# Performance work log

Hardware: AMD Instinct MI355X
Metric: run time of the kernel (lower is better)

## Reference

```python
import jax, jax.numpy as jnp
import numpy as np

B, E, NODE, M, N = 1024, 128, 128, 128, 512


def setup_inputs() -> dict:
    key = jax.random.key(0)
    k = jax.random.split(key, 7)
    s = 1.0 / np.sqrt(E)
    sn = 1.0 / np.sqrt(NODE)
    return {
        "h_v": jax.random.normal(k[0], (B, NODE, N), dtype=jnp.float32),
        "h_w": jax.random.normal(k[1], (B, NODE, N), dtype=jnp.float32),
        "e_vw": jax.random.normal(k[2], (B, E, N), dtype=jnp.float32),
        "W_e": jax.random.uniform(k[3], (M, E), jnp.float32, -s, s),
        "b_e": jax.random.uniform(k[4], (M,), jnp.float32, -s, s),
        "W_h": jax.random.uniform(k[5], (M, NODE), jnp.float32, -sn, sn),
        "b_h": jax.random.uniform(k[6], (M,), jnp.float32, -sn, sn),
    }


def reference(h_v, h_w, e_vw, W_e, b_e, W_h, b_h):
    # m_linear: message[:,:,n] = Linear_e(e_vw[:,:,n]) + Linear_h(h_w[:,:,n])
    # Vectorized over all nodes at once. Output: [B, M, N]
    msg = jnp.einsum('ben,me->bmn', e_vw, W_e) + jnp.einsum('bfn,mf->bmn', h_w, W_h)
    return msg + (b_e + b_h)[None, :, None]
```

## Files before the change

### kernel.cpp

```cpp
#include <hip/hip_runtime.h>


typedef __bf16 bf16x8 __attribute__((ext_vector_type(8)));
typedef float  f32x4  __attribute__((ext_vector_type(4)));

#define NDIM   512
#define MDIM   128
#define NCHUNK 64
#define KLD    264

__global__ __launch_bounds__(256) void msg_kernel(
    const float* __restrict__ h_w,
    const float* __restrict__ e_vw,
    const float* __restrict__ W_e,
    const float* __restrict__ b_e,
    const float* __restrict__ W_h,
    const float* __restrict__ b_h,
    float* __restrict__ out)
{
  __shared__ __align__(16) __bf16 Xs[NCHUNK][KLD];

  const int b    = blockIdx.x;
  const int tid  = threadIdx.x;
  const int lane = tid & 63;
  const int wave = tid >> 6;
  const int l15  = lane & 15;
  const int quad = lane >> 4;
  const int mbase = wave * 32;

  bf16x8 afrag[2][8];
#pragma unroll
  for (int mt = 0; mt < 2; ++mt) {
    const int m = mbase + mt * 16 + l15;
#pragma unroll
    for (int ks = 0; ks < 8; ++ks) {
      const int k0 = ks * 32 + quad * 8;
      const float* src = (k0 < 128) ? (W_e + m * 128 + k0)
                                    : (W_h + m * 128 + (k0 - 128));
      f32x4 lo = *(const f32x4*)(src);
      f32x4 hi = *(const f32x4*)(src + 4);
      bf16x8 f;
      f[0] = (__bf16)lo[0]; f[1] = (__bf16)lo[1];
      f[2] = (__bf16)lo[2]; f[3] = (__bf16)lo[3];
      f[4] = (__bf16)hi[0]; f[5] = (__bf16)hi[1];
      f[6] = (__bf16)hi[2]; f[7] = (__bf16)hi[3];
      afrag[mt][ks] = f;
    }
  }

  float bias[2][4];
#pragma unroll
  for (int mt = 0; mt < 2; ++mt)
#pragma unroll
    for (int r = 0; r < 4; ++r) {
      const int m = mbase + mt * 16 + quad * 4 + r;
      bias[mt][r] = b_e[m] + b_h[m];
    }

  const int krow0 = wave * 64;
  const float* src_base = (wave < 2)
      ? (e_vw + ((size_t)b * 128 + krow0) * NDIM)
      : (h_w  + ((size_t)b * 128 + (krow0 - 128)) * NDIM);

  float* outb = out + (size_t)b * MDIM * NDIM;
  const f32x4 fzero = {0.f, 0.f, 0.f, 0.f};

  for (int c = 0; c < 8; ++c) {
    const int n0 = c * NCHUNK;

#pragma unroll 2
    for (int g = 0; g < 8; ++g) {
      const float* p = src_base + (size_t)(g * 8) * NDIM + n0 + lane;
      float t[8];
#pragma unroll
      for (int j = 0; j < 8; ++j) t[j] = p[(size_t)j * NDIM];
      bf16x8 v;
#pragma unroll
      for (int j = 0; j < 8; ++j) v[j] = (__bf16)t[j];
      *(bf16x8*)&Xs[lane][krow0 + g * 8] = v;
    }
    __syncthreads();

    f32x4 acc[2][4];
#pragma unroll
    for (int mt = 0; mt < 2; ++mt)
#pragma unroll
      for (int nt = 0; nt < 4; ++nt)
        acc[mt][nt] = fzero;

#pragma unroll
    for (int ks = 0; ks < 8; ++ks) {
      bf16x8 bfrag[4];
#pragma unroll
      for (int nt = 0; nt < 4; ++nt)
        bfrag[nt] = *(const bf16x8*)&Xs[nt * 16 + l15][ks * 32 + quad * 8];
#pragma unroll
      for (int mt = 0; mt < 2; ++mt)
#pragma unroll
        for (int nt = 0; nt < 4; ++nt)
          acc[mt][nt] = __builtin_amdgcn_mfma_f32_16x16x32_bf16(
              afrag[mt][ks], bfrag[nt], acc[mt][nt], 0, 0, 0);
    }

#pragma unroll
    for (int mt = 0; mt < 2; ++mt)
#pragma unroll
      for (int nt = 0; nt < 4; ++nt)
#pragma unroll
        for (int r = 0; r < 4; ++r) {
          const int m = mbase + mt * 16 + quad * 4 + r;
          outb[(size_t)m * NDIM + n0 + nt * 16 + l15] = acc[mt][nt][r] + bias[mt][r];
        }
    __syncthreads();
  }
}

extern "C" void kernel_launch(void* const* d_in, const int* in_sizes, int n_in,
                              void* d_out, int out_size, void* d_ws, size_t ws_size,
                              hipStream_t stream) {
  const float* h_w  = (const float*)d_in[1];
  const float* e_vw = (const float*)d_in[2];
  const float* W_e  = (const float*)d_in[3];
  const float* b_e  = (const float*)d_in[4];
  const float* W_h  = (const float*)d_in[5];
  const float* b_h  = (const float*)d_in[6];
  float* out = (float*)d_out;

  msg_kernel<<<dim3(1024), dim3(256), 0, stream>>>(h_w, e_vw, W_e, b_e, W_h, b_h, out);
}
```

Before: 701.4 us.

## Swap MFMA operand roles: weights in swizzled LDS, activations loaded straight into registers

Restructures the kernel so that each 512-thread block handles a 128-column slice of one batch. Each lane loads its activation column directly from global memory into bf16 B fragments, with no LDS staging and no per-chunk barriers. The weight matrix is staged once per block into XOR-swizzled LDS to avoid bank conflicts, and output goes out through nontemporal stores. The grid grows to four times as many blocks for more parallelism. The trade-off is that every block now re-converts the full 64KB weight matrix, and each thread keeps 64 floats of activations live in registers.

```diff
diff --git a/kernel.cpp b/kernel.cpp
--- a/kernel.cpp
+++ b/kernel.cpp
@@ -4,12 +4,9 @@
 typedef __bf16 bf16x8 __attribute__((ext_vector_type(8)));
 typedef float  f32x4  __attribute__((ext_vector_type(4)));
 
-#define NDIM   512
-#define MDIM   128
-#define NCHUNK 64
-#define KLD    264
+#define NDIM 512
 
-__global__ __launch_bounds__(256) void msg_kernel(
+__global__ __launch_bounds__(512, 4) void msg_kernel(
     const float* __restrict__ h_w,
     const float* __restrict__ e_vw,
     const float* __restrict__ W_e,
@@ -18,100 +15,81 @@
     const float* __restrict__ b_h,
     float* __restrict__ out)
 {
-  __shared__ __align__(16) __bf16 Xs[NCHUNK][KLD];
+  __shared__ __align__(16) __bf16 Ws[128 * 256];
 
-  const int b    = blockIdx.x;
   const int tid  = threadIdx.x;
   const int lane = tid & 63;
   const int wave = tid >> 6;
   const int l15  = lane & 15;
   const int quad = lane >> 4;
-  const int mbase = wave * 32;
 
-  bf16x8 afrag[2][8];
+  const int b    = blockIdx.x >> 2;
+  const int nq   = blockIdx.x & 3;
+  const int ncol = nq * 128 + wave * 16 + l15;
+
+  const float* pe = e_vw + ((size_t)b * 128 + quad * 8) * NDIM + ncol;
+  const float* ph = h_w  + ((size_t)b * 128 + quad * 8) * NDIM + ncol;
+  float xs[8][8];
 #pragma unroll
-  for (int mt = 0; mt < 2; ++mt) {
-    const int m = mbase + mt * 16 + l15;
+  for (int s = 0; s < 4; ++s)
 #pragma unroll
-    for (int ks = 0; ks < 8; ++ks) {
-      const int k0 = ks * 32 + quad * 8;
-      const float* src = (k0 < 128) ? (W_e + m * 128 + k0)
-                                    : (W_h + m * 128 + (k0 - 128));
-      f32x4 lo = *(const f32x4*)(src);
-      f32x4 hi = *(const f32x4*)(src + 4);
-      bf16x8 f;
-      f[0] = (__bf16)lo[0]; f[1] = (__bf16)lo[1];
-      f[2] = (__bf16)lo[2]; f[3] = (__bf16)lo[3];
-      f[4] = (__bf16)hi[0]; f[5] = (__bf16)hi[1];
-      f[6] = (__bf16)hi[2]; f[7] = (__bf16)hi[3];
-      afrag[mt][ks] = f;
-    }
+    for (int j = 0; j < 8; ++j)
+      xs[s][j] = pe[(size_t)(s * 32 + j) * NDIM];
+#pragma unroll
+  for (int s = 0; s < 4; ++s)
+#pragma unroll
+    for (int j = 0; j < 8; ++j)
+      xs[4 + s][j] = ph[(size_t)(s * 32 + j) * NDIM];
+
+#pragma unroll
+  for (int i = 0; i < 4; ++i) {
+    const int A = i * 512 + tid;
+    const int m = A >> 4, a = A & 15;
+    f32x4 lo = *(const f32x4*)(W_e + A * 8);
+    f32x4 hi = *(const f32x4*)(W_e + A * 8 + 4);
+    bf16x8 v;
+    v[0]=(__bf16)lo[0]; v[1]=(__bf16)lo[1]; v[2]=(__bf16)lo[2]; v[3]=(__bf16)lo[3];
+    v[4]=(__bf16)hi[0]; v[5]=(__bf16)hi[1]; v[6]=(__bf16)hi[2]; v[7]=(__bf16)hi[3];
+    *(bf16x8*)&Ws[m * 256 + ((a ^ (m & 7)) * 8)] = v;
+  }
+#pragma unroll
+  for (int i = 0; i < 4; ++i) {
+    const int A = i * 512 + tid;
+    const int m = A >> 4, a = 16 + (A & 15);
+    f32x4 lo = *(const f32x4*)(W_h + A * 8);
+    f32x4 hi = *(const f32x4*)(W_h + A * 8 + 4);
+    bf16x8 v;
+    v[0]=(__bf16)lo[0]; v[1]=(__bf16)lo[1]; v[2]=(__bf16)lo[2]; v[3]=(__bf16)lo[3];
+    v[4]=(__bf16)hi[0]; v[5]=(__bf16)hi[1]; v[6]=(__bf16)hi[2]; v[7]=(__bf16)hi[3];
+    *(bf16x8*)&Ws[m * 256 + ((a ^ (m & 7)) * 8)] = v;
+  }
+  __syncthreads();
+
+  bf16x8 bfrag[8];
+#pragma unroll
+  for (int s = 0; s < 8; ++s) {
+#pragma unroll
+    for (int j = 0; j < 8; ++j) bfrag[s][j] = (__bf16)xs[s][j];
   }
 
-  float bias[2][4];
+  float* outp = out + (size_t)b * 128 * NDIM + ncol;
 #pragma unroll
-  for (int mt = 0; mt < 2; ++mt)
+  for (int mt = 0; mt < 8; ++mt) {
+    f32x4 acc = {0.f, 0.f, 0.f, 0.f};
+    const int m  = mt * 16 + l15;
+    const int sw = m & 7;
+#pragma unroll
+    for (int s = 0; s < 8; ++s) {
+      bf16x8 af = *(const bf16x8*)&Ws[m * 256 + (((s * 4 + quad) ^ sw) * 8)];
+      acc = __builtin_amdgcn_mfma_f32_16x16x32_bf16(af, bfrag[s], acc, 0, 0, 0);
+    }
+    f32x4 be = *(const f32x4*)(b_e + mt * 16 + quad * 4);
+    f32x4 bh = *(const f32x4*)(b_h + mt * 16 + quad * 4);
 #pragma unroll
     for (int r = 0; r < 4; ++r) {
-      const int m = mbase + mt * 16 + quad * 4 + r;
-      bias[mt][r] = b_e[m] + b_h[m];
+      __builtin_nontemporal_store(acc[r] + be[r] + bh[r],
+          outp + (size_t)(mt * 16 + quad * 4 + r) * NDIM);
     }
-
-  const int krow0 = wave * 64;
-  const float* src_base = (wave < 2)
-      ? (e_vw + ((size_t)b * 128 + krow0) * NDIM)
-      : (h_w  + ((size_t)b * 128 + (krow0 - 128)) * NDIM);
-
-  float* outb = out + (size_t)b * MDIM * NDIM;
-  const f32x4 fzero = {0.f, 0.f, 0.f, 0.f};
-
-  for (int c = 0; c < 8; ++c) {
-    const int n0 = c * NCHUNK;
-
-#pragma unroll 2
-    for (int g = 0; g < 8; ++g) {
-      const float* p = src_base + (size_t)(g * 8) * NDIM + n0 + lane;
-      float t[8];
-#pragma unroll
-      for (int j = 0; j < 8; ++j) t[j] = p[(size_t)j * NDIM];
-      bf16x8 v;
-#pragma unroll
-      for (int j = 0; j < 8; ++j) v[j] = (__bf16)t[j];
-      *(bf16x8*)&Xs[lane][krow0 + g * 8] = v;
-    }
-    __syncthreads();
-
-    f32x4 acc[2][4];
-#pragma unroll
-    for (int mt = 0; mt < 2; ++mt)
-#pragma unroll
-      for (int nt = 0; nt < 4; ++nt)
-        acc[mt][nt] = fzero;
-
-#pragma unroll
-    for (int ks = 0; ks < 8; ++ks) {
-      bf16x8 bfrag[4];
-#pragma unroll
-      for (int nt = 0; nt < 4; ++nt)
-        bfrag[nt] = *(const bf16x8*)&Xs[nt * 16 + l15][ks * 32 + quad * 8];
-#pragma unroll
-      for (int mt = 0; mt < 2; ++mt)
-#pragma unroll
-        for (int nt = 0; nt < 4; ++nt)
-          acc[mt][nt] = __builtin_amdgcn_mfma_f32_16x16x32_bf16(
-              afrag[mt][ks], bfrag[nt], acc[mt][nt], 0, 0, 0);
-    }
-
-#pragma unroll
-    for (int mt = 0; mt < 2; ++mt)
-#pragma unroll
-      for (int nt = 0; nt < 4; ++nt)
-#pragma unroll
-        for (int r = 0; r < 4; ++r) {
-          const int m = mbase + mt * 16 + quad * 4 + r;
-          outb[(size_t)m * NDIM + n0 + nt * 16 + l15] = acc[mt][nt][r] + bias[mt][r];
-        }
-    __syncthreads();
   }
 }
 
@@ -126,5 +104,6 @@
   const float* b_h  = (const float*)d_in[6];
   float* out = (float*)d_out;
 
-  msg_kernel<<<dim3(1024), dim3(256), 0, stream>>>(h_w, e_vw, W_e, b_e, W_h, b_h, out);
+  msg_kernel<<<dim3(1024 * 4), dim3(512), 0, stream>>>(
+      h_w, e_vw, W_e, b_e, W_h, b_h, out);
 }
```

Measured after the change: 753.1 us. +7.4%, slower.
